# Optimization experiments

Measured on AMD Instinct MI355X. Metric: run time of the kernel, lower is better.

## Reference

```python
import jax, jax.numpy as jnp
import numpy as np

B, N = 1, 768
C_A, C_S, C_Z = 768, 384, 128
H, C_HID, N_TRANS = 16, 48, 2
INF = 1e9
PNAMES = ['attn_s_ln_g', 'attn_ada_gate_w', 'attn_ada_gate_b', 'attn_ada_skip_w',
          'wq', 'bq', 'wk', 'wv', 'z_ln_g', 'z_ln_b', 'wb', 'wg', 'wo',
          'attn_out_gate_w', 'attn_out_gate_b',
          'tr_s_ln_g', 'tr_ada_gate_w', 'tr_ada_gate_b', 'tr_ada_skip_w',
          'tr_w1', 'tr_w2', 'tr_wo', 'tr_out_gate_w', 'tr_out_gate_b']


def _ln(x, eps=1e-5):
    mu = jnp.mean(x, axis=-1, keepdims=True)
    var = jnp.mean((x - mu) ** 2, axis=-1, keepdims=True)
    return (x - mu) * jax.lax.rsqrt(var + eps)


def _adaln(a, s, s_g, gate_w, gate_b, skip_w):
    # AF3 Algorithm 26 AdaLN: a <- LN(a, no affine); s <- LN(s, scale only)
    a_ln = _ln(a)
    s_ln = _ln(s) * s_g
    return jax.nn.sigmoid(s_ln @ gate_w + gate_b) * a_ln + s_ln @ skip_w


def setup_inputs() -> dict:
    key = jax.random.key(0)
    ks = iter(jax.random.split(key, 40))
    w = lambda *sh: jax.random.normal(next(ks), sh, jnp.float32) * 0.02
    return dict(
        a=jax.random.normal(next(ks), (B, N, C_A), jnp.float32),
        s=jax.random.normal(next(ks), (B, N, C_S), jnp.float32),
        z=jax.random.normal(next(ks), (B, N, N, C_Z), jnp.float32),
        mask=jnp.ones((B, N), jnp.int32),
        attn_s_ln_g=jnp.ones((C_S,), jnp.float32),
        attn_ada_gate_w=w(C_S, C_A),
        attn_ada_gate_b=jnp.zeros((C_A,), jnp.float32),
        attn_ada_skip_w=w(C_S, C_A),
        wq=w(C_A, H * C_HID), bq=jnp.zeros((H * C_HID,), jnp.float32),
        wk=w(C_A, H * C_HID), wv=w(C_A, H * C_HID),
        z_ln_g=jnp.ones((C_Z,), jnp.float32), z_ln_b=jnp.zeros((C_Z,), jnp.float32),
        wb=w(C_Z, H), wg=w(C_A, H * C_HID), wo=w(H * C_HID, C_A),
        attn_out_gate_w=w(C_S, C_A),
        attn_out_gate_b=jnp.full((C_A,), -2.0, jnp.float32),  # AdaLN-Zero bias init -2
        tr_s_ln_g=jnp.ones((C_S,), jnp.float32),
        tr_ada_gate_w=w(C_S, C_A),
        tr_ada_gate_b=jnp.zeros((C_A,), jnp.float32),
        tr_ada_skip_w=w(C_S, C_A),
        tr_w1=w(C_A, N_TRANS * C_A), tr_w2=w(C_A, N_TRANS * C_A),
        tr_wo=w(N_TRANS * C_A, C_A),
        tr_out_gate_w=w(C_S, C_A),
        tr_out_gate_b=jnp.full((C_A,), -2.0, jnp.float32),
    )


def _block(a, s, z, maskf, p):
    # --- AttentionPairBias (AF3 Alg 24), residual ---
    a_ln = _adaln(a, s, p['attn_s_ln_g'], p['attn_ada_gate_w'],
                  p['attn_ada_gate_b'], p['attn_ada_skip_w'])
    q = (a_ln @ p['wq'] + p['bq']).reshape(B, N, H, C_HID)
    k = (a_ln @ p['wk']).reshape(B, N, H, C_HID)
    v = (a_ln @ p['wv']).reshape(B, N, H, C_HID)
    pair_bias = (_ln(z) * p['z_ln_g'] + p['z_ln_b']) @ p['wb']  # [B,N,N,H]
    logits = jnp.einsum('bqhc,bkhc->bhqk', q, k) / np.float32(np.sqrt(C_HID))
    logits = logits + jnp.moveaxis(pair_bias, -1, 1)
    logits = logits + (maskf - 1.0)[:, None, None, :] * INF  # mask over keys
    attn = jax.nn.softmax(logits, axis=-1)
    o = jnp.einsum('bhqk,bkhc->bqhc', attn, v)
    g = jax.nn.sigmoid(a_ln @ p['wg']).reshape(B, N, H, C_HID)
    o = (o * g).reshape(B, N, H * C_HID) @ p['wo']
    o = jax.nn.sigmoid(s @ p['attn_out_gate_w'] + p['attn_out_gate_b']) * o
    a = a + o
    # --- ConditionedTransitionBlock (AF3 Alg 25, SwiGLU), residual ---
    t_ln = _adaln(a, s, p['tr_s_ln_g'], p['tr_ada_gate_w'],
                  p['tr_ada_gate_b'], p['tr_ada_skip_w'])
    hid = jax.nn.silu(t_ln @ p['tr_w1']) * (t_ln @ p['tr_w2'])
    t = jax.nn.sigmoid(s @ p['tr_out_gate_w'] + p['tr_out_gate_b']) * (hid @ p['tr_wo'])
    t = t * maskf[..., None]  # _mask_trans=True
    return a + t


def reference(a, s, z, mask, attn_s_ln_g, attn_ada_gate_w, attn_ada_gate_b,
              attn_ada_skip_w, wq, bq, wk, wv, z_ln_g, z_ln_b, wb, wg, wo,
              attn_out_gate_w, attn_out_gate_b, tr_s_ln_g, tr_ada_gate_w,
              tr_ada_gate_b, tr_ada_skip_w, tr_w1, tr_w2, tr_wo,
              tr_out_gate_w, tr_out_gate_b):
    p = dict(zip(PNAMES, (attn_s_ln_g, attn_ada_gate_w, attn_ada_gate_b,
                          attn_ada_skip_w, wq, bq, wk, wv, z_ln_g, z_ln_b, wb,
                          wg, wo, attn_out_gate_w, attn_out_gate_b, tr_s_ln_g,
                          tr_ada_gate_w, tr_ada_gate_b, tr_ada_skip_w, tr_w1,
                          tr_w2, tr_wo, tr_out_gate_w, tr_out_gate_b)))
    return _block(a, s, z, mask.astype(a.dtype), p)
```

## Files before the change

kernel.cpp:

```cpp
#include <hip/hip_runtime.h>
#include <hip/hip_bf16.h>
#include <stdint.h>


typedef __bf16 bf16x8 __attribute__((ext_vector_type(8)));
typedef float  f32x4  __attribute__((ext_vector_type(4)));

#define DEVI __device__ __forceinline__

DEVI uint16_t f2b(float f){ __hip_bfloat16 h = __float2bfloat16(f); return __builtin_bit_cast(uint16_t, h); }
DEVI float    b2f(uint16_t u){ return __bfloat162float(__builtin_bit_cast(__hip_bfloat16, u)); }
DEVI float    sigm(float x){ return 1.0f/(1.0f + __expf(-x)); }

DEVI f32x4 MFMA(uint4 a, uint4 b, f32x4 c){
  return __builtin_amdgcn_mfma_f32_16x16x32_bf16(
      __builtin_bit_cast(bf16x8, a), __builtin_bit_cast(bf16x8, b), c, 0, 0, 0);
}

DEVI void glds16(const void* g, void* l){
  __builtin_amdgcn_global_load_lds(
      (const __attribute__((address_space(1))) void*)g,
      (__attribute__((address_space(3))) void*)l, 16, 0, 0);
}

constexpr size_t SZ_BT_ADA   = (size_t)1536*384*2;
constexpr size_t OFF_BT_ADA_ATTN = 0;
constexpr size_t OFF_BT_ADA_TR   = OFF_BT_ADA_ATTN + SZ_BT_ADA;
constexpr size_t OFF_BT_OUTGATE  = OFF_BT_ADA_TR   + SZ_BT_ADA;
constexpr size_t OFF_BT_QKVG     = OFF_BT_OUTGATE  + SZ_BT_ADA;
constexpr size_t OFF_BT_WO       = OFF_BT_QKVG + (size_t)3072*768*2;
constexpr size_t OFF_BT_W12      = OFF_BT_WO   + (size_t)768*768*2;
constexpr size_t OFF_BT_TRWO     = OFF_BT_W12  + (size_t)3072*768*2;
constexpr size_t OFF_WBGT        = OFF_BT_TRWO + (size_t)768*1536*2;
constexpr size_t OFF_ZCOL        = OFF_WBGT + 4096;
constexpr size_t OFF_OGB         = OFF_ZCOL + 256;
constexpr size_t OFF_SBF         = OFF_OGB + 6144;
constexpr size_t OFF_SLNA        = OFF_SBF  + (size_t)768*384*2;
constexpr size_t OFF_SLNT        = OFF_SLNA + (size_t)768*384*2;
constexpr size_t OFF_GATEOUT     = OFF_SLNT + (size_t)768*384*2;
constexpr size_t OFF_GS          = OFF_GATEOUT + (size_t)768*1536*4;
constexpr size_t OFF_ALNBF       = OFF_GS + (size_t)768*1536*4;
constexpr size_t OFF_QKVGB       = OFF_ALNBF + (size_t)768*768*2;
constexpr size_t OFF_QP          = OFF_QKVGB + (size_t)768*3072*2;
constexpr size_t OFF_KP          = OFF_QP + (size_t)16*768*64*2;
constexpr size_t OFF_VT          = OFF_KP + (size_t)16*768*64*2;
constexpr size_t OFF_BIAS        = OFF_VT + (size_t)16*64*768*2;
constexpr size_t OFF_OBF         = OFF_BIAS + (size_t)16*768*768*2;
constexpr size_t OFF_AMID        = OFF_OBF + (size_t)768*768*2;

struct CvtArgs {
  const float* src[14];
  uint16_t*    dst[14];
  int K[14], N[14];
  int prefix[15];
};

__global__ __launch_bounds__(256) void k_cvt(CvtArgs a){
  int bid = blockIdx.x;
  int ti = 0;
  while (ti < 13 && bid >= a.prefix[ti+1]) ti++;
  int local = bid - a.prefix[ti];
  int K = a.K[ti], N = a.N[ti];
  int tN = N >> 5;
  int n0 = (local % tN) << 5, k0 = (local / tN) << 5;
  __shared__ float lds[32][33];
  const float* src = a.src[ti];
  uint16_t* dst = a.dst[ti];
  int t = threadIdx.x;
  int c = t & 31, r0 = t >> 5;
  #pragma unroll
  for (int i = 0; i < 4; i++){
    int kk = r0 + 8*i;
    lds[kk][c] = src[(size_t)(k0+kk)*N + n0 + c];
  }
  __syncthreads();
  #pragma unroll
  for (int i = 0; i < 4; i++){
    int nn = r0 + 8*i;
    dst[(size_t)(n0+nn)*K + k0 + c] = f2b(lds[c][nn]);
  }
}

__global__ __launch_bounds__(128) void k_prep(
    const float* s, const float* g_attn, const float* g_tr,
    const float* attn_ogb, const float* tr_ogb,
    const float* z_g, const float* z_b, const float* wb,
    uint16_t* s_bf, uint16_t* sln_a, uint16_t* sln_t,
    float* ogb, uint16_t* wbgt, float* zcol)
{
  int b = blockIdx.x, t = threadIdx.x;
  if (b < 768){
    const float* row = s + (size_t)b*384;
    float x0 = row[t], x1 = row[t+128], x2 = row[t+256];
    float sm = x0+x1+x2, sq = x0*x0+x1*x1+x2*x2;
    #pragma unroll
    for (int off = 32; off; off >>= 1){ sm += __shfl_xor(sm, off, 64); sq += __shfl_xor(sq, off, 64); }
    __shared__ float rs_[2], rq_[2];
    int w = t >> 6;
    if ((t & 63) == 0){ rs_[w] = sm; rq_[w] = sq; }
    __syncthreads();
    float S = rs_[0]+rs_[1], Q = rq_[0]+rq_[1];
    float mu = S * (1.f/384.f);
    float var = Q * (1.f/384.f) - mu*mu;
    float rstd = rsqrtf(var + 1e-5f);
    float xs[3] = {x0, x1, x2};
    #pragma unroll
    for (int i = 0; i < 3; i++){
      int ci = t + 128*i;
      float ln = (xs[i] - mu) * rstd;
      s_bf [(size_t)b*384 + ci] = f2b(xs[i]);
      sln_a[(size_t)b*384 + ci] = f2b(ln * g_attn[ci]);
      sln_t[(size_t)b*384 + ci] = f2b(ln * g_tr[ci]);
    }
  } else if (b == 768){
    for (int i = t; i < 1536; i += 128)
      ogb[i] = (i < 768) ? attn_ogb[i] : tr_ogb[i-768];
  } else {
    for (int i = t; i < 2048; i += 128){
      int h = i >> 7, c = i & 127;
      wbgt[i] = f2b(z_g[c] * wb[c*16 + h]);
    }
    if (t < 16){
      float cs = 0.f, cn = 0.f;
      for (int c = 0; c < 128; c++){ cs += z_g[c]*wb[c*16+t]; cn += z_b[c]*wb[c*16+t]; }
      zcol[t] = cs; zcol[16+t] = cn;
    }
  }
}

__global__ __launch_bounds__(256) void k_adaln2(
    const float* __restrict__ asrc, const float* __restrict__ gs,
    const float* __restrict__ gb, uint16_t* __restrict__ out)
{
  int b = blockIdx.x, t = threadIdx.x;
  const float* row = asrc + (size_t)b*768;
  float x0 = row[t], x1 = row[t+256], x2 = row[t+512];
  float sm = x0+x1+x2, sq = x0*x0+x1*x1+x2*x2;
  #pragma unroll
  for (int off = 32; off; off >>= 1){ sm += __shfl_xor(sm, off, 64); sq += __shfl_xor(sq, off, 64); }
  __shared__ float rs_[4], rq_[4];
  int w = t >> 6;
  if ((t & 63) == 0){ rs_[w] = sm; rq_[w] = sq; }
  __syncthreads();
  float S = rs_[0]+rs_[1]+rs_[2]+rs_[3], Q = rq_[0]+rq_[1]+rq_[2]+rq_[3];
  float mu = S*(1.f/768.f), var = Q*(1.f/768.f) - mu*mu, rstd = rsqrtf(var + 1e-5f);
  float xs[3] = {x0, x1, x2};
  #pragma unroll
  for (int i = 0; i < 3; i++){
    int c = t + 256*i;
    float g  = gs[(size_t)b*1536 + c];
    float sk = gs[(size_t)b*1536 + 768 + c];
    out[(size_t)b*768 + c] = f2b(sigm(g + gb[c]) * ((xs[i]-mu)*rstd) + sk);
  }
}

__global__ __launch_bounds__(256) void k_gemm(
    const uint16_t* __restrict__ A, const uint16_t* __restrict__ BT,
    int M, int N, int K,
    float* outF, uint16_t* outB, int mode,
    const float* bias, const float* gate, int gateLd, int gateOff,
    const float* resid, const int* mask)
{
  __shared__ uint16_t As[64*64], Bs[64*64];
  int t = threadIdx.x;
  int n0 = blockIdx.x*64, m0 = blockIdx.y*64;
  int w = t >> 6, lane = t & 63, mm = lane & 15, q = lane >> 4;
  int fc0 = 128*w + lane, fc1 = fc0 + 64;
  int r0 = fc0 >> 3, c0 = (fc0 & 7) ^ (r0 & 7);
  int r1 = fc1 >> 3, c1 = (fc1 & 7) ^ (r1 & 7);
  const uint16_t* gA0 = A  + (size_t)(m0 + r0)*K + c0*8;
  const uint16_t* gA1 = A  + (size_t)(m0 + r1)*K + c1*8;
  const uint16_t* gB0 = BT + (size_t)(n0 + r0)*K + c0*8;
  const uint16_t* gB1 = BT + (size_t)(n0 + r1)*K + c1*8;
  uint16_t* lA0 = As + (2*w + 0)*512;
  uint16_t* lA1 = As + (2*w + 1)*512;
  uint16_t* lB0 = Bs + (2*w + 0)*512;
  uint16_t* lB1 = Bs + (2*w + 1)*512;
  f32x4 zz = {0.f,0.f,0.f,0.f};
  f32x4 acc[4] = {zz, zz, zz, zz};
  int sw = mm & 7;
  for (int k0 = 0; k0 < K; k0 += 64){
    __syncthreads();
    glds16(gA0 + k0, lA0);
    glds16(gA1 + k0, lA1);
    glds16(gB0 + k0, lB0);
    glds16(gB1 + k0, lB1);
    __syncthreads();
    #pragma unroll
    for (int kc = 0; kc < 2; kc++){
      uint4 av = *(const uint4*)&As[(16*w + mm)*64 + ((kc*4 + q) ^ sw)*8];
      #pragma unroll
      for (int j = 0; j < 4; j++){
        uint4 bv = *(const uint4*)&Bs[(16*j + mm)*64 + ((kc*4 + q) ^ sw)*8];
        acc[j] = MFMA(av, bv, acc[j]);
      }
    }
  }
  #pragma unroll
  for (int j = 0; j < 4; j++){
    #pragma unroll
    for (int rr = 0; rr < 4; rr++){
      int row = m0 + 16*w + q*4 + rr;
      int col = n0 + 16*j + mm;
      float v = acc[j][rr];
      size_t oi = (size_t)row*N + col;
      if (mode == 0)      outF[oi] = v;
      else if (mode == 1) outB[oi] = f2b(v);
      else if (mode == 2) outF[oi] = sigm(v + bias[col]);
      else if (mode == 5) outF[oi] = resid[oi] + gate[(size_t)row*gateLd + gateOff + col]*v;
      else {
        float mf = (float)mask[row];
        outF[oi] = resid[oi] + mf * gate[(size_t)row*gateLd + gateOff + col] * v;
      }
    }
  }
}

__global__ __launch_bounds__(256) void k_zbias(
    const float* __restrict__ z, const uint16_t* __restrict__ wbgt_g,
    const float* __restrict__ zcol, uint16_t* __restrict__ bias_g)
{
  __shared__ uint16_t zb[64*128];
  __shared__ uint16_t wbt[16*128];
  __shared__ float mu_s[64], rs_s[64];
  __shared__ uint16_t Sout[16*72];
  int t = threadIdx.x;
  size_t P0 = (size_t)blockIdx.y*768 + (size_t)blockIdx.x*64;
  ((uint4*)wbt)[t] = ((const uint4*)wbgt_g)[t];
  int p = t >> 2, qq = t & 3;
  const float4* zp = (const float4*)(z + (P0 + p)*128) + qq*8;
  float s1 = 0.f, s2 = 0.f;
  uint32_t lb[16];
  #pragma unroll
  for (int it = 0; it < 8; it++){
    float4 v = zp[it];
    s1 += v.x + v.y + v.z + v.w;
    s2 += v.x*v.x + v.y*v.y + v.z*v.z + v.w*v.w;
    lb[2*it]   = (uint32_t)f2b(v.x) | ((uint32_t)f2b(v.y) << 16);
    lb[2*it+1] = (uint32_t)f2b(v.z) | ((uint32_t)f2b(v.w) << 16);
  }
  uint4* zb4 = (uint4*)zb;
  #pragma unroll
  for (int kk = 0; kk < 4; kk++)
    zb4[p*16 + qq*4 + kk] = ((uint4*)lb)[kk];
  s1 += __shfl_xor(s1, 1, 64); s1 += __shfl_xor(s1, 2, 64);
  s2 += __shfl_xor(s2, 1, 64); s2 += __shfl_xor(s2, 2, 64);
  if (qq == 0){
    float mu = s1 * (1.f/128.f);
    mu_s[p] = mu;
    rs_s[p] = rsqrtf(s2*(1.f/128.f) - mu*mu + 1e-5f);
  }
  __syncthreads();
  int w = t >> 6, lane = t & 63, hh = lane & 15, q = lane >> 4;
  float cs = zcol[hh], cn = zcol[16 + hh];
  f32x4 acc = {0.f, 0.f, 0.f, 0.f};
  const uint4* wbt4 = (const uint4*)wbt;
  #pragma unroll
  for (int kc = 0; kc < 4; kc++){
    uint4 av = zb4[(16*w + hh)*16 + kc*4 + q];
    uint4 bv = wbt4[hh*16 + kc*4 + q];
    acc = MFMA(av, bv, acc);
  }
  #pragma unroll
  for (int rr = 0; rr < 4; rr++){
    int pl = 16*w + q*4 + rr;
    float val = rs_s[pl]*(acc[rr] - mu_s[pl]*cs) + cn;
    Sout[hh*72 + pl] = f2b(val);
  }
  __syncthreads();
  int h2 = t >> 4, p2 = (t & 15)*4;
  uint2 v2 = *(uint2*)&Sout[h2*72 + p2];
  *(uint2*)(bias_g + (size_t)h2*589824 + P0 + p2) = v2;
}

__global__ __launch_bounds__(256) void k_trans(
    const uint16_t* __restrict__ qkvg, const float* __restrict__ bq,
    uint16_t* qp, uint16_t* kp, uint16_t* vt)
{
  int h = blockIdx.y, n0 = blockIdx.x*64, t = threadIdx.x;
  __shared__ uint16_t vbuf[64*72];
  int c = t & 63, r0 = t >> 6;
  const float scale = 0.14433756729740643f;
  for (int r = r0; r < 64; r += 4){
    size_t base = (size_t)(n0 + r)*3072;
    float qv = 0.f, kv = 0.f, vv = 0.f;
    if (c < 48){
      int cc = h*48 + c;
      qv = (b2f(qkvg[base + cc]) + bq[cc]) * scale;
      kv = b2f(qkvg[base + 768 + cc]);
      vv = b2f(qkvg[base + 1536 + cc]);
    }
    size_t oi = ((size_t)h*768 + n0 + r)*64 + c;
    qp[oi] = f2b(qv);
    kp[oi] = f2b(kv);
    vbuf[c*72 + r] = f2b(vv);
  }
  __syncthreads();
  int cc = t >> 2, rb = (t & 3)*16;
  uint16_t* dst = vt + ((size_t)h*64 + cc)*768 + n0 + rb;
  *(uint4*)dst       = *(uint4*)&vbuf[cc*72 + rb];
  *(uint4*)(dst + 8) = *(uint4*)&vbuf[cc*72 + rb + 8];
}

__global__ __launch_bounds__(256) void k_flash(
    const uint16_t* __restrict__ qp, const uint16_t* __restrict__ kp,
    const uint16_t* __restrict__ vt, const uint16_t* __restrict__ bias_g,
    const uint16_t* __restrict__ qkvg, const int* __restrict__ mask,
    uint16_t* __restrict__ obf)
{
  __shared__ uint16_t Qs[64*72], Ks[64*72], Vs[64*72], Ps[64*72];
  __shared__ float mk[768];
  int t = threadIdx.x;
  int q0 = blockIdx.x*64, h = blockIdx.y;
  int w = t >> 6, lane = t & 63, mm = lane & 15, q = lane >> 4;
  {
    int row = t >> 2, c = t & 3;
    const uint4* src = (const uint4*)(qp + ((size_t)h*768 + q0 + row)*64) + c*2;
    *(uint4*)&Qs[row*72 + c*16]     = src[0];
    *(uint4*)&Qs[row*72 + c*16 + 8] = src[1];
    mk[t] = (float)mask[t]; mk[t+256] = (float)mask[t+256]; mk[t+512] = (float)mask[t+512];
  }
  f32x4 zz = {0.f,0.f,0.f,0.f};
  f32x4 o0 = zz, o1 = zz, o2 = zz;
  f32x4 m_i = {-1e30f,-1e30f,-1e30f,-1e30f};
  f32x4 l_i = zz;
  const uint16_t* bias_h = bias_g + (size_t)h*589824;
  for (int kt = 0; kt < 12; kt++){
    __syncthreads();
    {
      int row = t >> 2, c = t & 3;
      const uint4* ks = (const uint4*)(kp + ((size_t)h*768 + kt*64 + row)*64) + c*2;
      *(uint4*)&Ks[row*72 + c*16]     = ks[0];
      *(uint4*)&Ks[row*72 + c*16 + 8] = ks[1];
      const uint4* vs = (const uint4*)(vt + ((size_t)h*64 + row)*768 + kt*64) + c*2;
      *(uint4*)&Vs[row*72 + c*16]     = vs[0];
      *(uint4*)&Vs[row*72 + c*16 + 8] = vs[1];
    }
    __syncthreads();
    f32x4 s[4] = {zz, zz, zz, zz};
    #pragma unroll
    for (int kc = 0; kc < 2; kc++){
      uint4 av = *(const uint4*)&Qs[(16*w + mm)*72 + kc*32 + q*8];
      #pragma unroll
      for (int j = 0; j < 4; j++){
        uint4 bv = *(const uint4*)&Ks[(16*j + mm)*72 + kc*32 + q*8];
        s[j] = MFMA(av, bv, s[j]);
      }
    }
    int srow = q0 + 16*w + q*4;
    #pragma unroll
    for (int j = 0; j < 4; j++){
      int scol = kt*64 + 16*j + mm;
      float mt = (mk[scol] - 1.f)*1e9f;
      #pragma unroll
      for (int rr = 0; rr < 4; rr++)
        s[j][rr] += b2f(bias_h[(size_t)(srow+rr)*768 + scol]) + mt;
    }
    f32x4 tm = s[0];
    #pragma unroll
    for (int j = 1; j < 4; j++)
      #pragma unroll
      for (int rr = 0; rr < 4; rr++) tm[rr] = fmaxf(tm[rr], s[j][rr]);
    #pragma unroll
    for (int off = 1; off < 16; off <<= 1)
      #pragma unroll
      for (int rr = 0; rr < 4; rr++) tm[rr] = fmaxf(tm[rr], __shfl_xor(tm[rr], off, 64));
    f32x4 mnew, alpha, rsum = zz;
    #pragma unroll
    for (int rr = 0; rr < 4; rr++){
      mnew[rr] = fmaxf(m_i[rr], tm[rr]);
      alpha[rr] = __expf(m_i[rr] - mnew[rr]);
    }
    #pragma unroll
    for (int j = 0; j < 4; j++)
      #pragma unroll
      for (int rr = 0; rr < 4; rr++){
        s[j][rr] = __expf(s[j][rr] - mnew[rr]);
        rsum[rr] += s[j][rr];
      }
    #pragma unroll
    for (int off = 1; off < 16; off <<= 1)
      #pragma unroll
      for (int rr = 0; rr < 4; rr++) rsum[rr] += __shfl_xor(rsum[rr], off, 64);
    #pragma unroll
    for (int rr = 0; rr < 4; rr++){
      l_i[rr] = l_i[rr]*alpha[rr] + rsum[rr];
      o0[rr] *= alpha[rr]; o1[rr] *= alpha[rr]; o2[rr] *= alpha[rr];
      m_i[rr] = mnew[rr];
    }
    #pragma unroll
    for (int j = 0; j < 4; j++)
      #pragma unroll
      for (int rr = 0; rr < 4; rr++)
        Ps[(16*w + q*4 + rr)*72 + 16*j + mm] = f2b(s[j][rr]);
    __syncthreads();
    #pragma unroll
    for (int kc = 0; kc < 2; kc++){
      uint4 av = *(const uint4*)&Ps[(16*w + mm)*72 + kc*32 + q*8];
      uint4 bv0 = *(const uint4*)&Vs[(mm)*72      + kc*32 + q*8];
      uint4 bv1 = *(const uint4*)&Vs[(16+mm)*72   + kc*32 + q*8];
      uint4 bv2 = *(const uint4*)&Vs[(32+mm)*72   + kc*32 + q*8];
      o0 = MFMA(av, bv0, o0);
      o1 = MFMA(av, bv1, o1);
      o2 = MFMA(av, bv2, o2);
    }
  }
  f32x4 inv;
  #pragma unroll
  for (int rr = 0; rr < 4; rr++) inv[rr] = 1.f / l_i[rr];
  #pragma unroll
  for (int j = 0; j < 3; j++){
    f32x4 ov = (j == 0) ? o0 : (j == 1) ? o1 : o2;
    int col = 16*j + mm;
    #pragma unroll
    for (int rr = 0; rr < 4; rr++){
      int row = q0 + 16*w + q*4 + rr;
      float g = b2f(qkvg[(size_t)row*3072 + 2304 + h*48 + col]);
      obf[(size_t)row*768 + h*48 + col] = f2b(ov[rr]*inv[rr]*sigm(g));
    }
  }
}

__global__ __launch_bounds__(256) void k_silu(const uint16_t* __restrict__ h12, uint16_t* __restrict__ hid){
  int idx4 = blockIdx.x*256 + threadIdx.x;
  int row = idx4 / 384;
  int c4 = (idx4 % 384)*4;
  const uint16_t* p1 = h12 + (size_t)row*3072 + c4;
  const uint16_t* p2 = p1 + 1536;
  uint16_t o[4];
  #pragma unroll
  for (int i = 0; i < 4; i++){
    float x1 = b2f(p1[i]), x2 = b2f(p2[i]);
    o[i] = f2b(x1*sigm(x1)*x2);
  }
  *(uint2*)(hid + (size_t)row*1536 + c4) = *(uint2*)o;
}

extern "C" void kernel_launch(void* const* d_in, const int* in_sizes, int n_in,
                              void* d_out, int out_size, void* d_ws, size_t ws_size,
                              hipStream_t stream)
{
  const float* a            = (const float*)d_in[0];
  const float* s            = (const float*)d_in[1];
  const float* z            = (const float*)d_in[2];
  const int*   mask         = (const int*)  d_in[3];
  const float* attn_s_ln_g  = (const float*)d_in[4];
  const float* attn_gate_w  = (const float*)d_in[5];
  const float* attn_gate_b  = (const float*)d_in[6];
  const float* attn_skip_w  = (const float*)d_in[7];
  const float* wq           = (const float*)d_in[8];
  const float* bq           = (const float*)d_in[9];
  const float* wk           = (const float*)d_in[10];
  const float* wv           = (const float*)d_in[11];
  const float* z_ln_g       = (const float*)d_in[12];
  const float* z_ln_b       = (const float*)d_in[13];
  const float* wb           = (const float*)d_in[14];
  const float* wg           = (const float*)d_in[15];
  const float* wo           = (const float*)d_in[16];
  const float* attn_og_w    = (const float*)d_in[17];
  const float* attn_og_b    = (const float*)d_in[18];
  const float* tr_s_ln_g    = (const float*)d_in[19];
  const float* tr_gate_w    = (const float*)d_in[20];
  const float* tr_gate_b    = (const float*)d_in[21];
  const float* tr_skip_w    = (const float*)d_in[22];
  const float* tr_w1        = (const float*)d_in[23];
  const float* tr_w2        = (const float*)d_in[24];
  const float* tr_wo        = (const float*)d_in[25];
  const float* tr_og_w      = (const float*)d_in[26];
  const float* tr_og_b      = (const float*)d_in[27];

  char* wsb = (char*)d_ws;
  uint16_t* BTa   = (uint16_t*)(wsb + OFF_BT_ADA_ATTN);
  uint16_t* BTt   = (uint16_t*)(wsb + OFF_BT_ADA_TR);
  uint16_t* BTo   = (uint16_t*)(wsb + OFF_BT_OUTGATE);
  uint16_t* BTq   = (uint16_t*)(wsb + OFF_BT_QKVG);
  uint16_t* BTwo  = (uint16_t*)(wsb + OFF_BT_WO);
  uint16_t* BTw12 = (uint16_t*)(wsb + OFF_BT_W12);
  uint16_t* BTtw  = (uint16_t*)(wsb + OFF_BT_TRWO);
  uint16_t* WBGT  = (uint16_t*)(wsb + OFF_WBGT);
  float*    ZCOL  = (float*)   (wsb + OFF_ZCOL);
  float*    OGB   = (float*)   (wsb + OFF_OGB);
  uint16_t* SBF   = (uint16_t*)(wsb + OFF_SBF);
  uint16_t* SLNA  = (uint16_t*)(wsb + OFF_SLNA);
  uint16_t* SLNT  = (uint16_t*)(wsb + OFF_SLNT);
  float*    GATEOUT=(float*)   (wsb + OFF_GATEOUT);
  float*    GS    = (float*)   (wsb + OFF_GS);
  uint16_t* ALNBF = (uint16_t*)(wsb + OFF_ALNBF);
  uint16_t* QKVGB = (uint16_t*)(wsb + OFF_QKVGB);
  uint16_t* QP    = (uint16_t*)(wsb + OFF_QP);
  uint16_t* KP    = (uint16_t*)(wsb + OFF_KP);
  uint16_t* VT    = (uint16_t*)(wsb + OFF_VT);
  uint16_t* BIASB = (uint16_t*)(wsb + OFF_BIAS);
  uint16_t* OBF   = (uint16_t*)(wsb + OFF_OBF);
  float*    AMID  = (float*)   (wsb + OFF_AMID);
  uint16_t* HIDBF = (uint16_t*)(wsb + OFF_BIAS);
  float*    OUTF  = (float*)d_out;

  CvtArgs ca;
  const float* srcs[14] = {attn_gate_w, attn_skip_w, tr_gate_w, tr_skip_w,
                           attn_og_w, tr_og_w, wq, wk, wv, wg, wo, tr_w1, tr_w2, tr_wo};
  uint16_t* dsts[14] = {BTa, BTa + (size_t)768*384, BTt, BTt + (size_t)768*384,
                        BTo, BTo + (size_t)768*384,
                        BTq, BTq + (size_t)768*768, BTq + (size_t)2*768*768, BTq + (size_t)3*768*768,
                        BTwo, BTw12, BTw12 + (size_t)1536*768, BTtw};
  int Ks[14] = {384,384,384,384,384,384, 768,768,768,768,768, 768,768, 1536};
  int Ns[14] = {768,768,768,768,768,768, 768,768,768,768,768, 1536,1536, 768};
  int tiles[14] = {288,288,288,288,288,288, 576,576,576,576,576, 1152,1152, 1152};
  int pre = 0;
  for (int i = 0; i < 14; i++){
    ca.src[i] = srcs[i]; ca.dst[i] = dsts[i]; ca.K[i] = Ks[i]; ca.N[i] = Ns[i];
    ca.prefix[i] = pre; pre += tiles[i];
  }
  ca.prefix[14] = pre;

  k_cvt<<<pre, 256, 0, stream>>>(ca);
  k_prep<<<770, 128, 0, stream>>>(s, attn_s_ln_g, tr_s_ln_g, attn_og_b, tr_og_b,
                                  z_ln_g, z_ln_b, wb, SBF, SLNA, SLNT, OGB, WBGT, ZCOL);

  k_gemm<<<dim3(24,12), 256, 0, stream>>>(SBF, BTo, 768, 1536, 384,
      GATEOUT, nullptr, 2, OGB, nullptr, 0, 0, nullptr, nullptr);
  k_gemm<<<dim3(24,12), 256, 0, stream>>>(SLNA, BTa, 768, 1536, 384,
      GS, nullptr, 0, nullptr, nullptr, 0, 0, nullptr, nullptr);
  k_adaln2<<<768, 256, 0, stream>>>(a, GS, attn_gate_b, ALNBF);
  k_gemm<<<dim3(48,12), 256, 0, stream>>>(ALNBF, BTq, 768, 3072, 768,
      nullptr, QKVGB, 1, nullptr, nullptr, 0, 0, nullptr, nullptr);

  k_zbias<<<dim3(12,768), 256, 0, stream>>>(z, WBGT, ZCOL, BIASB);
  k_trans<<<dim3(12,16), 256, 0, stream>>>(QKVGB, bq, QP, KP, VT);
  k_flash<<<dim3(12,16), 256, 0, stream>>>(QP, KP, VT, BIASB, QKVGB, mask, OBF);
  k_gemm<<<dim3(12,12), 256, 0, stream>>>(OBF, BTwo, 768, 768, 768,
      AMID, nullptr, 5, nullptr, GATEOUT, 1536, 0, a, nullptr);

  k_gemm<<<dim3(24,12), 256, 0, stream>>>(SLNT, BTt, 768, 1536, 384,
      GS, nullptr, 0, nullptr, nullptr, 0, 0, nullptr, nullptr);
  k_adaln2<<<768, 256, 0, stream>>>(AMID, GS, tr_gate_b, ALNBF);
  k_gemm<<<dim3(48,12), 256, 0, stream>>>(ALNBF, BTw12, 768, 3072, 768,
      nullptr, QKVGB, 1, nullptr, nullptr, 0, 0, nullptr, nullptr);
  k_silu<<<1152, 256, 0, stream>>>(QKVGB, HIDBF);
  k_gemm<<<dim3(12,12), 256, 0, stream>>>(HIDBF, BTtw, 768, 768, 1536,
      OUTF, nullptr, 4, nullptr, GATEOUT, 1536, 768, AMID, mask);
}
```

Baseline: 635.3 us.

## Add 128x128 GEMM tiles, batch s-projection GEMMs, stage flash bias in LDS

Adds a 128x128-tile GEMM core with a 2x2 warp layout and 4x4 MFMA accumulators per warp. It is used for the two N=3072 projections, to raise data reuse per tile. The three s-conditioned projections (out-gate, attention AdaLN, transition AdaLN) now run in one batched launch over blockIdx.z, with a separate GST buffer so the transition projection can run early. The flash kernel also loads each 64x64 pair-bias tile into LDS with coalesced vector loads instead of scattered per-element global reads. Costs: more LDS and registers per block, fewer blocks for the large GEMMs, and the new tile drops the XOR swizzle, which may cause LDS bank conflicts.

```diff
diff --git a/kernel.cpp b/kernel.cpp
--- a/kernel.cpp
+++ b/kernel.cpp
@@ -39,7 +39,8 @@
 constexpr size_t OFF_SLNT        = OFF_SLNA + (size_t)768*384*2;
 constexpr size_t OFF_GATEOUT     = OFF_SLNT + (size_t)768*384*2;
 constexpr size_t OFF_GS          = OFF_GATEOUT + (size_t)768*1536*4;
-constexpr size_t OFF_ALNBF       = OFF_GS + (size_t)768*1536*4;
+constexpr size_t OFF_GST         = OFF_GS   + (size_t)768*1536*4;
+constexpr size_t OFF_ALNBF       = OFF_GST  + (size_t)768*1536*4;
 constexpr size_t OFF_QKVGB       = OFF_ALNBF + (size_t)768*768*2;
 constexpr size_t OFF_QP          = OFF_QKVGB + (size_t)768*3072*2;
 constexpr size_t OFF_KP          = OFF_QP + (size_t)16*768*64*2;
@@ -154,11 +155,100 @@
   }
 }
 
+DEVI void g128_core(const uint16_t* __restrict__ A, const uint16_t* __restrict__ BT,
+                    int K, int N, int m0, int n0,
+                    float* outF, uint16_t* outB, int mode, const float* bias)
+{
+  __shared__ uint16_t As[128*64], Bs[128*64];
+  int t = threadIdx.x;
+  int w = t >> 6, lane = t & 63, mm = lane & 15, q = lane >> 4;
+  int rowblk = (w >> 1)*64, colblk = (w & 1)*64;
+  const uint16_t* gA[4]; const uint16_t* gB[4];
+  uint16_t* lA[4]; uint16_t* lB[4];
+  #pragma unroll
+  for (int s2 = 0; s2 < 4; s2++){
+    int ci = 256*w + 64*s2 + lane;
+    int r = ci >> 3, c = ci & 7;
+    gA[s2] = A  + (size_t)(m0 + r)*K + c*8;
+    gB[s2] = BT + (size_t)(n0 + r)*K + c*8;
+    lA[s2] = As + (size_t)(256*w + 64*s2)*8;
+    lB[s2] = Bs + (size_t)(256*w + 64*s2)*8;
+  }
+  f32x4 zz = {0.f,0.f,0.f,0.f};
+  f32x4 acc[4][4];
+  #pragma unroll
+  for (int i = 0; i < 4; i++)
+    #pragma unroll
+    for (int j = 0; j < 4; j++) acc[i][j] = zz;
+  for (int k0 = 0; k0 < K; k0 += 64){
+    __syncthreads();
+    #pragma unroll
+    for (int s2 = 0; s2 < 4; s2++){
+      glds16(gA[s2] + k0, lA[s2]);
+      glds16(gB[s2] + k0, lB[s2]);
+    }
+    __syncthreads();
+    #pragma unroll
+    for (int kc = 0; kc < 2; kc++){
+      uint4 av[4], bv[4];
+      #pragma unroll
+      for (int i = 0; i < 4; i++)
+        av[i] = *(const uint4*)&As[(rowblk + 16*i + mm)*64 + kc*32 + q*8];
+      #pragma unroll
+      for (int j = 0; j < 4; j++)
+        bv[j] = *(const uint4*)&Bs[(colblk + 16*j + mm)*64 + kc*32 + q*8];
+      #pragma unroll
+      for (int i = 0; i < 4; i++)
+        #pragma unroll
+        for (int j = 0; j < 4; j++)
+          acc[i][j] = MFMA(av[i], bv[j], acc[i][j]);
+    }
+  }
+  #pragma unroll
+  for (int i = 0; i < 4; i++){
+    #pragma unroll
+    for (int j = 0; j < 4; j++){
+      #pragma unroll
+      for (int rr = 0; rr < 4; rr++){
+        int row = m0 + rowblk + 16*i + q*4 + rr;
+        int col = n0 + colblk + 16*j + mm;
+        float v = acc[i][j][rr];
+        size_t oi = (size_t)row*N + col;
+        if (mode == 0)      outF[oi] = v;
+        else if (mode == 1) outB[oi] = f2b(v);
+        else                outF[oi] = sigm(v + bias[col]);
+      }
+    }
+  }
+}
+
+__global__ __launch_bounds__(256) void k_gemm128(
+    const uint16_t* __restrict__ A, const uint16_t* __restrict__ BT,
+    int K, int N, float* outF, uint16_t* outB, int mode, const float* bias)
+{
+  g128_core(A, BT, K, N, blockIdx.y*128, blockIdx.x*128, outF, outB, mode, bias);
+}
+
+__global__ __launch_bounds__(256) void k_sfused(
+    const uint16_t* __restrict__ SBF, const uint16_t* __restrict__ SLNA,
+    const uint16_t* __restrict__ SLNT,
+    const uint16_t* __restrict__ BTo, const uint16_t* __restrict__ BTa,
+    const uint16_t* __restrict__ BTt,
+    float* GATEOUT, float* GS, float* GST, const float* OGB)
+{
+  int zi = blockIdx.z;
+  const uint16_t* A  = (zi == 0) ? SBF : (zi == 1) ? SLNA : SLNT;
+  const uint16_t* BT = (zi == 0) ? BTo : (zi == 1) ? BTa  : BTt;
+  float* out         = (zi == 0) ? GATEOUT : (zi == 1) ? GS : GST;
+  int mode           = (zi == 0) ? 2 : 0;
+  g128_core(A, BT, 384, 1536, blockIdx.y*128, blockIdx.x*128, out, nullptr, mode, OGB);
+}
+
 __global__ __launch_bounds__(256) void k_gemm(
     const uint16_t* __restrict__ A, const uint16_t* __restrict__ BT,
     int M, int N, int K,
-    float* outF, uint16_t* outB, int mode,
-    const float* bias, const float* gate, int gateLd, int gateOff,
+    float* outF, int mode,
+    const float* gate, int gateLd, int gateOff,
     const float* resid, const int* mask)
 {
   __shared__ uint16_t As[64*64], Bs[64*64];
@@ -204,10 +294,7 @@
       int col = n0 + 16*j + mm;
       float v = acc[j][rr];
       size_t oi = (size_t)row*N + col;
-      if (mode == 0)      outF[oi] = v;
-      else if (mode == 1) outB[oi] = f2b(v);
-      else if (mode == 2) outF[oi] = sigm(v + bias[col]);
-      else if (mode == 5) outF[oi] = resid[oi] + gate[(size_t)row*gateLd + gateOff + col]*v;
+      if (mode == 5) outF[oi] = resid[oi] + gate[(size_t)row*gateLd + gateOff + col]*v;
       else {
         float mf = (float)mask[row];
         outF[oi] = resid[oi] + mf * gate[(size_t)row*gateLd + gateOff + col] * v;
@@ -308,7 +395,7 @@
     const uint16_t* __restrict__ qkvg, const int* __restrict__ mask,
     uint16_t* __restrict__ obf)
 {
-  __shared__ uint16_t Qs[64*72], Ks[64*72], Vs[64*72], Ps[64*72];
+  __shared__ uint16_t Qs[64*72], Ks[64*72], Vs[64*72], Ps[64*72], Bb[64*72];
   __shared__ float mk[768];
   int t = threadIdx.x;
   int q0 = blockIdx.x*64, h = blockIdx.y;
@@ -335,6 +422,9 @@
       const uint4* vs = (const uint4*)(vt + ((size_t)h*64 + row)*768 + kt*64) + c*2;
       *(uint4*)&Vs[row*72 + c*16]     = vs[0];
       *(uint4*)&Vs[row*72 + c*16 + 8] = vs[1];
+      const uint4* bs = (const uint4*)(bias_h + (size_t)(q0 + row)*768 + kt*64) + c*2;
+      *(uint4*)&Bb[row*72 + c*16]     = bs[0];
+      *(uint4*)&Bb[row*72 + c*16 + 8] = bs[1];
     }
     __syncthreads();
     f32x4 s[4] = {zz, zz, zz, zz};
@@ -347,14 +437,14 @@
         s[j] = MFMA(av, bv, s[j]);
       }
     }
-    int srow = q0 + 16*w + q*4;
     #pragma unroll
     for (int j = 0; j < 4; j++){
       int scol = kt*64 + 16*j + mm;
       float mt = (mk[scol] - 1.f)*1e9f;
+      int lr = 16*w + q*4;
       #pragma unroll
       for (int rr = 0; rr < 4; rr++)
-        s[j][rr] += b2f(bias_h[(size_t)(srow+rr)*768 + scol]) + mt;
+        s[j][rr] += b2f(Bb[(lr+rr)*72 + 16*j + mm]) + mt;
     }
     f32x4 tm = s[0];
     #pragma unroll
@@ -485,6 +575,7 @@
   uint16_t* SLNT  = (uint16_t*)(wsb + OFF_SLNT);
   float*    GATEOUT=(float*)   (wsb + OFF_GATEOUT);
   float*    GS    = (float*)   (wsb + OFF_GS);
+  float*    GST   = (float*)   (wsb + OFF_GST);
   uint16_t* ALNBF = (uint16_t*)(wsb + OFF_ALNBF);
   uint16_t* QKVGB = (uint16_t*)(wsb + OFF_QKVGB);
   uint16_t* QP    = (uint16_t*)(wsb + OFF_QP);
@@ -517,26 +608,22 @@
   k_prep<<<770, 128, 0, stream>>>(s, attn_s_ln_g, tr_s_ln_g, attn_og_b, tr_og_b,
                                   z_ln_g, z_ln_b, wb, SBF, SLNA, SLNT, OGB, WBGT, ZCOL);
 
-  k_gemm<<<dim3(24,12), 256, 0, stream>>>(SBF, BTo, 768, 1536, 384,
-      GATEOUT, nullptr, 2, OGB, nullptr, 0, 0, nullptr, nullptr);
-  k_gemm<<<dim3(24,12), 256, 0, stream>>>(SLNA, BTa, 768, 1536, 384,
-      GS, nullptr, 0, nullptr, nullptr, 0, 0, nullptr, nullptr);
+  k_sfused<<<dim3(12,6,3), 256, 0, stream>>>(SBF, SLNA, SLNT, BTo, BTa, BTt,
+                                             GATEOUT, GS, GST, OGB);
   k_adaln2<<<768, 256, 0, stream>>>(a, GS, attn_gate_b, ALNBF);
-  k_gemm<<<dim3(48,12), 256, 0, stream>>>(ALNBF, BTq, 768, 3072, 768,
-      nullptr, QKVGB, 1, nullptr, nullptr, 0, 0, nullptr, nullptr);
+  k_gemm128<<<dim3(24,6), 256, 0, stream>>>(ALNBF, BTq, 768, 3072,
+      nullptr, QKVGB, 1, nullptr);
 
   k_zbias<<<dim3(12,768), 256, 0, stream>>>(z, WBGT, ZCOL, BIASB);
   k_trans<<<dim3(12,16), 256, 0, stream>>>(QKVGB, bq, QP, KP, VT);
   k_flash<<<dim3(12,16), 256, 0, stream>>>(QP, KP, VT, BIASB, QKVGB, mask, OBF);
   k_gemm<<<dim3(12,12), 256, 0, stream>>>(OBF, BTwo, 768, 768, 768,
-      AMID, nullptr, 5, nullptr, GATEOUT, 1536, 0, a, nullptr);
-
-  k_gemm<<<dim3(24,12), 256, 0, stream>>>(SLNT, BTt, 768, 1536, 384,
-      GS, nullptr, 0, nullptr, nullptr, 0, 0, nullptr, nullptr);
-  k_adaln2<<<768, 256, 0, stream>>>(AMID, GS, tr_gate_b, ALNBF);
-  k_gemm<<<dim3(48,12), 256, 0, stream>>>(ALNBF, BTw12, 768, 3072, 768,
-      nullptr, QKVGB, 1, nullptr, nullptr, 0, 0, nullptr, nullptr);
+      AMID, 5, GATEOUT, 1536, 0, a, nullptr);
+
+  k_adaln2<<<768, 256, 0, stream>>>(AMID, GST, tr_gate_b, ALNBF);
+  k_gemm128<<<dim3(24,6), 256, 0, stream>>>(ALNBF, BTw12, 768, 3072,
+      nullptr, QKVGB, 1, nullptr);
   k_silu<<<1152, 256, 0, stream>>>(QKVGB, HIDBF);
   k_gemm<<<dim3(12,12), 256, 0, stream>>>(HIDBF, BTtw, 768, 768, 1536,
-      OUTF, nullptr, 4, nullptr, GATEOUT, 1536, 768, AMID, mask);
-}
+      OUTF, 4, GATEOUT, 1536, 768, AMID, mask);
+}
```

After: 644.5 us. Within noise of the previous version (+1.5%).
